# Kernel optimization log

Hardware: AMD Instinct MI355X
Metric: run time of the kernel (lower is better)

The kernel has to match this reference:

```python
import jax, jax.numpy as jnp
import numpy as np

N_NODES = 20000
N_EDGES = 100000
D_IN = 768
NEG_SLOPE = 0.2  # DGL GATConv default


def _gat_layer(x, W, attn_l, attn_r, bias, src, dst, num_heads, head_dim, use_elu):
    N = x.shape[0]
    z = (x @ W).reshape(N, num_heads, head_dim)          # [N,H,D]
    el = jnp.sum(z * attn_l, axis=-1)                    # [N,H]
    er = jnp.sum(z * attn_r, axis=-1)                    # [N,H]
    e = jax.nn.leaky_relu(el[src] + er[dst], NEG_SLOPE)  # [E,H]
    # segment softmax over incoming edges of each dst node
    m = jax.ops.segment_max(e, dst, num_segments=N)      # [N,H] (-inf for isolated nodes, never gathered)
    ex = jnp.exp(e - m[dst])                             # [E,H]
    denom = jax.ops.segment_sum(ex, dst, num_segments=N) # [N,H]
    alpha = ex / denom[dst]                              # [E,H]
    msg = alpha[:, :, None] * z[src]                     # [E,H,D]
    out = jax.ops.segment_sum(msg, dst, num_segments=N)  # [N,H,D]
    out = out + z                                        # identity residual (in == H*D)
    out = out + bias.reshape(1, num_heads, head_dim)
    if use_elu:
        out = jax.nn.elu(out)
    return out.reshape(N, num_heads * head_dim)


def setup_inputs() -> dict:
    key = jax.random.key(0)
    ks = jax.random.split(key, 16)
    node_features = jax.random.normal(ks[0], (N_NODES, D_IN), dtype=jnp.float32)
    src = jax.random.randint(ks[1], (N_EDGES,), 0, N_NODES)
    dst = jax.random.randint(ks[2], (N_EDGES,), 0, N_NODES)
    s = 1.0 / np.sqrt(D_IN)
    inp = {"node_features": node_features, "src": src, "dst": dst}
    # layers 0,1: H=12, D=64; layer 2: H=1, D=768
    heads = [(12, 64), (12, 64), (1, 768)]
    for i, (H, D) in enumerate(heads):
        inp[f"W{i}"] = jax.random.normal(ks[3 + 4 * i], (D_IN, H * D), dtype=jnp.float32) * s
        inp[f"al{i}"] = jax.random.normal(ks[4 + 4 * i], (H, D), dtype=jnp.float32) * s
        inp[f"ar{i}"] = jax.random.normal(ks[5 + 4 * i], (H, D), dtype=jnp.float32) * s
        inp[f"b{i}"] = jnp.zeros((H * D,), dtype=jnp.float32)
    return inp


def reference(node_features, W0, al0, ar0, b0, W1, al1, ar1, b1, W2, al2, ar2, b2, src, dst):
    x = _gat_layer(node_features, W0, al0, ar0, b0, src, dst, 12, 64, True)
    x = _gat_layer(x, W1, al1, ar1, b1, src, dst, 12, 64, True)
    x = _gat_layer(x, W2, al2, ar2, b2, src, dst, 1, 768, False)
    return x
```

## Files before the change

kernel.cpp:

```cpp
#include <hip/hip_runtime.h>
#include <cstdint>
#include <cstddef>

#define DINL __device__ __forceinline__

typedef __attribute__((ext_vector_type(8))) short bf16x8;
typedef __attribute__((ext_vector_type(4))) float f32x4;

DINL unsigned f32_ord(float f) {
    unsigned u = __float_as_uint(f);
    return (u & 0x80000000u) ? ~u : (u | 0x80000000u);
}
DINL float ord_f32(unsigned v) {
    return (v & 0x80000000u) ? __uint_as_float(v & 0x7FFFFFFFu)
                             : __uint_as_float(~v);
}

DINL unsigned short f2bf(float f) {
    unsigned u = __float_as_uint(f);
    unsigned r = u + 0x7FFFu + ((u >> 16) & 1u);
    return (unsigned short)(r >> 16);
}
DINL float bf2f(unsigned short h) { return __uint_as_float((unsigned)h << 16); }

#define GLOAD_LDS16(g, l)                                                     \
    __builtin_amdgcn_global_load_lds(                                         \
        (const __attribute__((address_space(1))) void*)(g),                   \
        (__attribute__((address_space(3))) void*)(l), 16, 0, 0)

__global__ void decompose_a(const float* __restrict__ x,
                            unsigned short* __restrict__ hi,
                            unsigned short* __restrict__ lo,
                            int Nrows, int Mpad) {
    int i4 = blockIdx.x * blockDim.x + threadIdx.x;
    int total = Mpad * 192;
    if (i4 >= total) return;
    int row = i4 / 192;
    float4 v = (row < Nrows) ? ((const float4*)x)[i4]
                             : make_float4(0.f, 0.f, 0.f, 0.f);
    ushort4 h, l;
    h.x = f2bf(v.x); l.x = f2bf(v.x - bf2f(h.x));
    h.y = f2bf(v.y); l.y = f2bf(v.y - bf2f(h.y));
    h.z = f2bf(v.z); l.z = f2bf(v.z - bf2f(h.z));
    h.w = f2bf(v.w); l.w = f2bf(v.w - bf2f(h.w));
    ((ushort4*)hi)[i4] = h;
    ((ushort4*)lo)[i4] = l;
}

__global__ __launch_bounds__(256) void decompose_bT(const float* __restrict__ W,
                                                    unsigned short* __restrict__ hiT,
                                                    unsigned short* __restrict__ loT) {
    __shared__ float tile[64][65];
    int k0 = blockIdx.x * 64, n0 = blockIdx.y * 64;
    int t = threadIdx.x;
#pragma unroll
    for (int i = 0; i < 16; ++i) {
        int idx = t + i * 256;
        int r = idx >> 6, c = idx & 63;
        tile[r][c] = W[(size_t)(k0 + r) * 768 + n0 + c];
    }
    __syncthreads();
#pragma unroll
    for (int i = 0; i < 16; ++i) {
        int idx = t + i * 256;
        int r = idx >> 6, c = idx & 63;
        float v = tile[c][r];
        unsigned short h = f2bf(v);
        hiT[(size_t)(n0 + r) * 768 + k0 + c] = h;
        loT[(size_t)(n0 + r) * 768 + k0 + c] = f2bf(v - bf2f(h));
    }
}

__global__ __launch_bounds__(256) void gemm_fused_bf16(
        const unsigned short* __restrict__ Ahi, const unsigned short* __restrict__ Alo,
        const unsigned short* __restrict__ BThi, const unsigned short* __restrict__ BTlo,
        float* __restrict__ C,
        const float* __restrict__ attl, const float* __restrict__ attr,
        float* __restrict__ el, float* __restrict__ er,
        int Nrows, int do_attn) {
    constexpr int K = 768, NC = 768, BKK = 32;
    __shared__ __align__(16) unsigned short AsH[128 * BKK];
    __shared__ __align__(16) unsigned short AsL[128 * BKK];
    __shared__ __align__(16) unsigned short BsH[128 * BKK];
    __shared__ __align__(16) unsigned short BsL[128 * BKK];
    const int t = threadIdx.x, w = t >> 6, l = t & 63;
    const int m0 = blockIdx.x * 128, n0 = blockIdx.y * 128;
    const int wr = w >> 1, wc = w & 1;

    f32x4 acc[4][4] = {};

    const int srow = w * 16 + (l >> 2);
    const int scol = (l & 3) * 8;
    const int kr = (l >> 4) * 8;

    for (int k0 = 0; k0 < K; k0 += BKK) {
        __syncthreads();
#pragma unroll
        for (int c = 0; c < 2; ++c) {
            const size_t ga = (size_t)(m0 + c * 64 + srow) * K + k0 + scol;
            const size_t gb = (size_t)(n0 + c * 64 + srow) * K + k0 + scol;
            const int lofs = (c * 64 + w * 16) * BKK;
            GLOAD_LDS16(Ahi + ga, AsH + lofs);
            GLOAD_LDS16(Alo + ga, AsL + lofs);
            GLOAD_LDS16(BThi + gb, BsH + lofs);
            GLOAD_LDS16(BTlo + gb, BsL + lofs);
        }
        __syncthreads();

        bf16x8 fbh[4], fbl[4];
#pragma unroll
        for (int j = 0; j < 4; ++j) {
            const int row = (wc * 64 + j * 16 + (l & 15)) * BKK + kr;
            fbh[j] = *(const bf16x8*)&BsH[row];
            fbl[j] = *(const bf16x8*)&BsL[row];
        }
#pragma unroll
        for (int i = 0; i < 4; ++i) {
            const int row = (wr * 64 + i * 16 + (l & 15)) * BKK + kr;
            bf16x8 fah = *(const bf16x8*)&AsH[row];
            bf16x8 fal = *(const bf16x8*)&AsL[row];
#pragma unroll
            for (int j = 0; j < 4; ++j) {
                acc[i][j] = __builtin_amdgcn_mfma_f32_16x16x32_bf16(fah, fbh[j], acc[i][j], 0, 0, 0);
                acc[i][j] = __builtin_amdgcn_mfma_f32_16x16x32_bf16(fah, fbl[j], acc[i][j], 0, 0, 0);
                acc[i][j] = __builtin_amdgcn_mfma_f32_16x16x32_bf16(fal, fbh[j], acc[i][j], 0, 0, 0);
            }
        }
    }

    const int crow = m0 + wr * 64 + (l >> 4) * 4;
    const int ccol = n0 + wc * 64 + (l & 15);
#pragma unroll
    for (int i = 0; i < 4; ++i)
#pragma unroll
        for (int j = 0; j < 4; ++j)
#pragma unroll
            for (int r = 0; r < 4; ++r)
                C[(size_t)(crow + i * 16 + r) * NC + ccol + j * 16] = acc[i][j][r];

    if (do_attn) {
        const int h = blockIdx.y * 2 + wc;
        float alc[4], arc[4];
#pragma unroll
        for (int j = 0; j < 4; ++j) {
            alc[j] = attl[h * 64 + (l & 15) + j * 16];
            arc[j] = attr[h * 64 + (l & 15) + j * 16];
        }
#pragma unroll
        for (int i = 0; i < 4; ++i)
#pragma unroll
            for (int r = 0; r < 4; ++r) {
                float sl = 0.f, sr = 0.f;
#pragma unroll
                for (int j = 0; j < 4; ++j) {
                    sl += acc[i][j][r] * alc[j];
                    sr += acc[i][j][r] * arc[j];
                }
#pragma unroll
                for (int o = 1; o < 16; o <<= 1) {
                    sl += __shfl_xor(sl, o);
                    sr += __shfl_xor(sr, o);
                }
                int row = crow + i * 16 + r;
                if ((l & 15) == 0 && row < Nrows) {
                    el[row * 12 + h] = sl;
                    er[row * 12 + h] = sr;
                }
            }
    }
}

__global__ __launch_bounds__(256) void el_er_kernel(const float* __restrict__ z,
                                                    const float* __restrict__ al,
                                                    const float* __restrict__ ar,
                                                    float* __restrict__ el,
                                                    float* __restrict__ er,
                                                    int N, int H, int Dh) {
    int wid = (blockIdx.x * 256 + threadIdx.x) >> 6;
    int lane = threadIdx.x & 63;
    if (wid >= N * H) return;
    int n = wid / H, h = wid % H;
    const float* zr = z + (size_t)n * (H * Dh) + h * Dh;
    const float* alr = al + h * Dh;
    const float* arr = ar + h * Dh;
    float sl = 0.f, sr = 0.f;
    for (int d = lane; d < Dh; d += 64) {
        float zv = zr[d];
        sl += zv * alr[d];
        sr += zv * arr[d];
    }
#pragma unroll
    for (int o = 32; o; o >>= 1) {
        sl += __shfl_down(sl, o);
        sr += __shfl_down(sr, o);
    }
    if (lane == 0) { el[wid] = sl; er[wid] = sr; }
}

__global__ void init_mdenom(unsigned* __restrict__ m, float* __restrict__ denom, int n) {
    int i = blockIdx.x * blockDim.x + threadIdx.x;
    if (i < n) { m[i] = 0u; denom[i] = 0.f; }
}

__global__ void edge_e_kernel(const int* __restrict__ src, const int* __restrict__ dst,
                              const float* __restrict__ el, const float* __restrict__ er,
                              float* __restrict__ e, unsigned* __restrict__ m,
                              int E, int H) {
    int i = blockIdx.x * blockDim.x + threadIdx.x;
    if (i >= E * H) return;
    int ed = i / H, h = i - ed * H;
    int s = src[ed], d = dst[ed];
    float v = el[s * H + h] + er[d * H + h];
    v = (v >= 0.f) ? v : 0.2f * v;
    e[i] = v;
    atomicMax(&m[d * H + h], f32_ord(v));
}

__global__ void edge_ex_kernel(const int* __restrict__ dst,
                               float* __restrict__ e, const unsigned* __restrict__ m,
                               float* __restrict__ denom, int E, int H) {
    int i = blockIdx.x * blockDim.x + threadIdx.x;
    if (i >= E * H) return;
    int ed = i / H, h = i - ed * H;
    int d = dst[ed];
    float x = expf(e[i] - ord_f32(m[d * H + h]));
    e[i] = x;
    atomicAdd(&denom[d * H + h], x);
}

__global__ void csr_zero(int* __restrict__ counts, int* __restrict__ cursor, int N) {
    int i = blockIdx.x * blockDim.x + threadIdx.x;
    if (i < N) { counts[i] = 0; cursor[i] = 0; }
}

__global__ void csr_count(const int* __restrict__ dst, int* __restrict__ counts, int E) {
    int i = blockIdx.x * blockDim.x + threadIdx.x;
    if (i < E) atomicAdd(&counts[dst[i]], 1);
}

__global__ __launch_bounds__(1024) void csr_scan(const int* __restrict__ counts,
                                                 int* __restrict__ offsets, int N, int E) {
    __shared__ int part[1024];
    const int t = threadIdx.x;
    const int CH = (N + 1023) / 1024;
    const int base = t * CH;
    int s = 0;
    for (int i = 0; i < CH; ++i) {
        int idx = base + i;
        if (idx < N) s += counts[idx];
    }
    part[t] = s;
    __syncthreads();
    for (int o = 1; o < 1024; o <<= 1) {
        int v = (t >= o) ? part[t - o] : 0;
        __syncthreads();
        part[t] += v;
        __syncthreads();
    }
    int run = (t > 0) ? part[t - 1] : 0;
    for (int i = 0; i < CH; ++i) {
        int idx = base + i;
        if (idx < N) { offsets[idx] = run; run += counts[idx]; }
    }
    if (t == 1023) offsets[N] = E;
}

__global__ void csr_scatter(const int* __restrict__ src, const int* __restrict__ dst,
                            const int* __restrict__ offsets, int* __restrict__ cursor,
                            int* __restrict__ perm, int* __restrict__ psrc, int E) {
    int e = blockIdx.x * blockDim.x + threadIdx.x;
    if (e >= E) return;
    int d = dst[e];
    int pos = offsets[d] + atomicAdd(&cursor[d], 1);
    perm[pos] = e;
    psrc[pos] = src[e];
}

__global__ __launch_bounds__(256) void aggregate_csr(const int* __restrict__ offsets,
                                                     const int* __restrict__ perm,
                                                     const int* __restrict__ psrc,
                                                     const float* __restrict__ z,
                                                     const float* __restrict__ ex,
                                                     const float* __restrict__ denom,
                                                     const float* __restrict__ bias,
                                                     float* __restrict__ out,
                                                     unsigned short* __restrict__ nAhi,
                                                     unsigned short* __restrict__ nAlo,
                                                     int N, int Mpad, int H, int Dh,
                                                     int use_elu, int mode) {
    int d = (blockIdx.x * 256 + threadIdx.x) >> 6;
    int lane = threadIdx.x & 63;
    int limit = mode ? Mpad : N;
    if (d >= limit) return;

    if (d >= N) {
        ushort4 zz = {0, 0, 0, 0};
#pragma unroll
        for (int q = 0; q < 3; ++q) {
            ((ushort4*)nAhi)[(size_t)d * 192 + lane + 64 * q] = zz;
            ((ushort4*)nAlo)[(size_t)d * 192 + lane + 64 * q] = zz;
        }
        return;
    }

    float inv_den = 0.f;
    if (lane < H) inv_den = 1.0f / denom[d * H + lane];

    const float4* zd = (const float4*)(z + (size_t)d * 768);
    const float4* bv = (const float4*)bias;
    float4 acc[3];
#pragma unroll
    for (int q = 0; q < 3; ++q) {
        float4 a = zd[lane + 64 * q];
        float4 b = bv[lane + 64 * q];
        acc[q] = make_float4(a.x + b.x, a.y + b.y, a.z + b.z, a.w + b.w);
    }

    const int beg = offsets[d], end = offsets[d + 1];
    for (int p = beg; p < end; ++p) {
        int e = perm[p];
        int s = psrc[p];
        float alpha = 0.f;
        if (lane < H) alpha = ex[(size_t)e * H + lane] * inv_den;
        const float4* zs = (const float4*)(z + (size_t)s * 768);
#pragma unroll
        for (int q = 0; q < 3; ++q) {
            int idx = lane + 64 * q;
            int h = (4 * idx) / Dh;
            float a = __shfl(alpha, h);
            float4 zv = zs[idx];
            acc[q].x += a * zv.x;
            acc[q].y += a * zv.y;
            acc[q].z += a * zv.z;
            acc[q].w += a * zv.w;
        }
    }

#pragma unroll
    for (int q = 0; q < 3; ++q) {
        float4 v = acc[q];
        if (use_elu) {
            v.x = v.x > 0.f ? v.x : expm1f(v.x);
            v.y = v.y > 0.f ? v.y : expm1f(v.y);
            v.z = v.z > 0.f ? v.z : expm1f(v.z);
            v.w = v.w > 0.f ? v.w : expm1f(v.w);
        }
        if (mode) {
            ushort4 h4, l4;
            h4.x = f2bf(v.x); l4.x = f2bf(v.x - bf2f(h4.x));
            h4.y = f2bf(v.y); l4.y = f2bf(v.y - bf2f(h4.y));
            h4.z = f2bf(v.z); l4.z = f2bf(v.z - bf2f(h4.z));
            h4.w = f2bf(v.w); l4.w = f2bf(v.w - bf2f(h4.w));
            ((ushort4*)nAhi)[(size_t)d * 192 + lane + 64 * q] = h4;
            ((ushort4*)nAlo)[(size_t)d * 192 + lane + 64 * q] = l4;
        } else {
            ((float4*)(out + (size_t)d * 768))[lane + 64 * q] = v;
        }
    }
}

static void run_layer(const float* W, const float* al, const float* ar,
                      const float* bias, const int* src, const int* dst,
                      const int* offsets, const int* perm, const int* psrc,
                      unsigned short* Ahi, unsigned short* Alo,
                      unsigned short* BThi, unsigned short* BTlo,
                      float* z, float* out, float* ebuf, float* el, float* er,
                      unsigned* m, float* denom,
                      int N, int Mpad, int E, int H, int Dh, bool use_elu, int mode,
                      hipStream_t stream) {
    decompose_bT<<<dim3(12, 12), 256, 0, stream>>>(W, BThi, BTlo);
    gemm_fused_bf16<<<dim3(Mpad / 128, 6), 256, 0, stream>>>(
        Ahi, Alo, BThi, BTlo, z, al, ar, el, er, N, H == 12 ? 1 : 0);
    if (H != 12)
        el_er_kernel<<<(N * H * 64 + 255) / 256, 256, 0, stream>>>(z, al, ar, el, er, N, H, Dh);
    init_mdenom<<<(N * H + 255) / 256, 256, 0, stream>>>(m, denom, N * H);
    edge_e_kernel<<<(E * H + 255) / 256, 256, 0, stream>>>(src, dst, el, er, ebuf, m, E, H);
    edge_ex_kernel<<<(E * H + 255) / 256, 256, 0, stream>>>(dst, ebuf, m, denom, E, H);
    int waves = mode ? Mpad : N;
    aggregate_csr<<<(waves * 64 + 255) / 256, 256, 0, stream>>>(
        offsets, perm, psrc, z, ebuf, denom, bias, out, Ahi, Alo,
        N, Mpad, H, Dh, use_elu ? 1 : 0, mode);
}

extern "C" void kernel_launch(void* const* d_in, const int* in_sizes, int n_in,
                              void* d_out, int out_size, void* d_ws, size_t ws_size,
                              hipStream_t stream) {
    const float* x0 = (const float*)d_in[0];
    const int* src = (const int*)d_in[1];
    const int* dst = (const int*)d_in[2];
    const float* W[3]  = {(const float*)d_in[3], (const float*)d_in[7],  (const float*)d_in[11]};
    const float* al[3] = {(const float*)d_in[4], (const float*)d_in[8],  (const float*)d_in[12]};
    const float* ar[3] = {(const float*)d_in[5], (const float*)d_in[9],  (const float*)d_in[13]};
    const float* bs[3] = {(const float*)d_in[6], (const float*)d_in[10], (const float*)d_in[14]};

    const int N = in_sizes[0] / 768;
    const int E = in_sizes[1];
    const int Mpad = ((N + 127) / 128) * 128;

    char* p = (char*)d_ws;
    const size_t FP = (size_t)Mpad * 768 * sizeof(float);
    const size_t BF = (size_t)Mpad * 768 * sizeof(unsigned short);
    float* z = (float*)p;                 p += FP;
    unsigned short* Ahi = (unsigned short*)p;  p += BF;
    unsigned short* Alo = (unsigned short*)p;  p += BF;
    unsigned short* BThi = (unsigned short*)p; p += (size_t)768 * 768 * 2;
    unsigned short* BTlo = (unsigned short*)p; p += (size_t)768 * 768 * 2;
    float* ebuf = (float*)p;              p += (size_t)E * 12 * sizeof(float);
    float* el = (float*)p;                p += (size_t)N * 12 * sizeof(float);
    float* er = (float*)p;                p += (size_t)N * 12 * sizeof(float);
    unsigned* m = (unsigned*)p;           p += (size_t)N * 12 * sizeof(unsigned);
    float* denom = (float*)p;             p += (size_t)N * 12 * sizeof(float);
    int* counts = (int*)p;                p += (size_t)N * sizeof(int);
    int* cursor = (int*)p;                p += (size_t)N * sizeof(int);
    int* offsets = (int*)p;               p += (size_t)(N + 4) * sizeof(int);
    int* perm = (int*)p;                  p += (size_t)E * sizeof(int);
    int* psrc = (int*)p;                  p += (size_t)E * sizeof(int);

    csr_zero<<<(N + 255) / 256, 256, 0, stream>>>(counts, cursor, N);
    csr_count<<<(E + 255) / 256, 256, 0, stream>>>(dst, counts, E);
    csr_scan<<<1, 1024, 0, stream>>>(counts, offsets, N, E);
    csr_scatter<<<(E + 255) / 256, 256, 0, stream>>>(src, dst, offsets, cursor, perm, psrc, E);

    decompose_a<<<(Mpad * 192 + 255) / 256, 256, 0, stream>>>(x0, Ahi, Alo, N, Mpad);

    run_layer(W[0], al[0], ar[0], bs[0], src, dst, offsets, perm, psrc,
              Ahi, Alo, BThi, BTlo, z, nullptr, ebuf, el, er, m, denom,
              N, Mpad, E, 12, 64, true, 1, stream);
    run_layer(W[1], al[1], ar[1], bs[1], src, dst, offsets, perm, psrc,
              Ahi, Alo, BThi, BTlo, z, nullptr, ebuf, el, er, m, denom,
              N, Mpad, E, 12, 64, true, 1, stream);
    run_layer(W[2], al[2], ar[2], bs[2], src, dst, offsets, perm, psrc,
              Ahi, Alo, BThi, BTlo, z, (float*)d_out, ebuf, el, er, m, denom,
              N, Mpad, E, 1, 768, false, 0, stream);
}
```

Measured before the change: 725.6 us.

## Double-buffer LDS tiles in fused bf16 GEMM to overlap loads with MFMA

Converts the GEMM main loop to a two-stage LDS ping-pong. The next K-tile is issued with direct global-to-LDS loads while MFMAs run on the current tile, and each iteration ends with a single wait plus barrier instead of two barriers. It also raises wave priority around the MFMA block. This doubles LDS use from 32KB to 64KB per block, which may cut occupancy. The barrier at the end of each iteration also relies on every wave having finished its LDS reads before the buffer is overwritten.

```diff
diff --git a/kernel.cpp b/kernel.cpp
--- a/kernel.cpp
+++ b/kernel.cpp
@@ -78,11 +78,11 @@
         const float* __restrict__ attl, const float* __restrict__ attr,
         float* __restrict__ el, float* __restrict__ er,
         int Nrows, int do_attn) {
-    constexpr int K = 768, NC = 768, BKK = 32;
-    __shared__ __align__(16) unsigned short AsH[128 * BKK];
-    __shared__ __align__(16) unsigned short AsL[128 * BKK];
-    __shared__ __align__(16) unsigned short BsH[128 * BKK];
-    __shared__ __align__(16) unsigned short BsL[128 * BKK];
+    constexpr int K = 768, NC = 768, BKK = 32, NT = K / BKK;
+    __shared__ __align__(16) unsigned short AsH[2][128 * BKK];
+    __shared__ __align__(16) unsigned short AsL[2][128 * BKK];
+    __shared__ __align__(16) unsigned short BsH[2][128 * BKK];
+    __shared__ __align__(16) unsigned short BsL[2][128 * BKK];
     const int t = threadIdx.x, w = t >> 6, l = t & 63;
     const int m0 = blockIdx.x * 128, n0 = blockIdx.y * 128;
     const int wr = w >> 1, wc = w & 1;
@@ -93,32 +93,40 @@
     const int scol = (l & 3) * 8;
     const int kr = (l >> 4) * 8;
 
-    for (int k0 = 0; k0 < K; k0 += BKK) {
-        __syncthreads();
+    auto stage = [&](int buf, int k0) {
 #pragma unroll
         for (int c = 0; c < 2; ++c) {
             const size_t ga = (size_t)(m0 + c * 64 + srow) * K + k0 + scol;
             const size_t gb = (size_t)(n0 + c * 64 + srow) * K + k0 + scol;
             const int lofs = (c * 64 + w * 16) * BKK;
-            GLOAD_LDS16(Ahi + ga, AsH + lofs);
-            GLOAD_LDS16(Alo + ga, AsL + lofs);
-            GLOAD_LDS16(BThi + gb, BsH + lofs);
-            GLOAD_LDS16(BTlo + gb, BsL + lofs);
-        }
-        __syncthreads();
+            GLOAD_LDS16(Ahi + ga, &AsH[buf][lofs]);
+            GLOAD_LDS16(Alo + ga, &AsL[buf][lofs]);
+            GLOAD_LDS16(BThi + gb, &BsH[buf][lofs]);
+            GLOAD_LDS16(BTlo + gb, &BsL[buf][lofs]);
+        }
+    };
+
+    stage(0, 0);
+    asm volatile("s_waitcnt vmcnt(0)" ::: "memory");
+    __builtin_amdgcn_s_barrier();
+
+    for (int tt = 0; tt < NT; ++tt) {
+        const int cur = tt & 1;
+        if (tt < NT - 1) stage(cur ^ 1, (tt + 1) * BKK);
 
         bf16x8 fbh[4], fbl[4];
 #pragma unroll
         for (int j = 0; j < 4; ++j) {
             const int row = (wc * 64 + j * 16 + (l & 15)) * BKK + kr;
-            fbh[j] = *(const bf16x8*)&BsH[row];
-            fbl[j] = *(const bf16x8*)&BsL[row];
-        }
+            fbh[j] = *(const bf16x8*)&BsH[cur][row];
+            fbl[j] = *(const bf16x8*)&BsL[cur][row];
+        }
+        __builtin_amdgcn_s_setprio(1);
 #pragma unroll
         for (int i = 0; i < 4; ++i) {
             const int row = (wr * 64 + i * 16 + (l & 15)) * BKK + kr;
-            bf16x8 fah = *(const bf16x8*)&AsH[row];
-            bf16x8 fal = *(const bf16x8*)&AsL[row];
+            bf16x8 fah = *(const bf16x8*)&AsH[cur][row];
+            bf16x8 fal = *(const bf16x8*)&AsL[cur][row];
 #pragma unroll
             for (int j = 0; j < 4; ++j) {
                 acc[i][j] = __builtin_amdgcn_mfma_f32_16x16x32_bf16(fah, fbh[j], acc[i][j], 0, 0, 0);
@@ -126,6 +134,10 @@
                 acc[i][j] = __builtin_amdgcn_mfma_f32_16x16x32_bf16(fal, fbh[j], acc[i][j], 0, 0, 0);
             }
         }
+        __builtin_amdgcn_s_setprio(0);
+
+        asm volatile("s_waitcnt vmcnt(0)" ::: "memory");
+        __builtin_amdgcn_s_barrier();
     }
 
     const int crow = m0 + wr * 64 + (l >> 4) * 4;
```

Result: slower. 743.6 us (+2.5%).
